# Optimization experiments

Hardware: AMD Instinct MI355X
Metric: run time of the kernel (lower is better)

The kernel has to match this reference:

```python
import jax, jax.numpy as jnp
import numpy as np

BS, NV, MF, MT, NP, K, NR = 8, 16, 16, 16, 8, 3, 12
H, NOUT = 64, 64


def setup_inputs() -> dict:
    key = jax.random.key(0)
    ks = jax.random.split(key, 8)
    rel_index = jax.random.uniform(ks[0], (BS, NV, MF, MT, NP, K, NR), jnp.float32)
    source_embed = jax.random.normal(ks[1], (BS, NV, MT, MF, H), jnp.float32)
    s = jax.random.normal(ks[2], (BS, NV, NOUT), jnp.float32)
    # relation matrices: W[0] is fixed all-ones, rest xavier_uniform(gain=1.414)
    bound = 1.414 * np.sqrt(6.0 / (H + H))
    W0 = jnp.ones((1, H, H), jnp.float32)
    Wr = jax.random.uniform(ks[3], (NR - 1, H, H), jnp.float32, -bound, bound)
    Wstack = jnp.concatenate([W0, Wr], axis=0)  # (NR, H, H)
    lb = 1.0 / np.sqrt(H + NOUT)
    lin_w = jax.random.uniform(ks[4], (1, H + NOUT), jnp.float32, -lb, lb)
    lin_b = jax.random.uniform(ks[5], (1,), jnp.float32, -lb, lb)
    ob = 1.0 / np.sqrt(H)
    out_w = jax.random.uniform(ks[6], (NOUT, H), jnp.float32, -ob, ob)
    out_b = jax.random.uniform(ks[7], (NOUT,), jnp.float32, -ob, ob)
    return dict(rel_index=rel_index, source_embed=source_embed, s=s,
                Wstack=Wstack, lin_w=lin_w, lin_b=lin_b, out_w=out_w, out_b=out_b)


def reference(rel_index, source_embed, s, Wstack, lin_w, lin_b, out_w, out_b):
    # Original: rels = (rel_index @ Wflat).view(..., K, h, h); W = prod over K (ELEMENTWISE);
    # einsum 'bvtfpdd,bvtfd->bvtfpd' takes the DIAGONAL of the (h,h) block.
    # diag(elementwise prod) == prod of diags, so only diag(W_r) is needed -> same math,
    # avoids materializing the (b,v,f,t,p,K,h,h) tensor.
    diag = jnp.diagonal(Wstack, axis1=-2, axis2=-1)              # (nr, h)
    rels_d = jnp.einsum('bvftpkr,rd->bvftpkd', rel_index, diag)  # (b,v,f,t,p,K,h)
    Wd = jnp.prod(rels_d, axis=-2)                               # prod over K -> (b,v,f,t,p,h)
    Wd = jnp.swapaxes(Wd, 2, 3)                                  # permute -> (b,v,t,f,p,h)
    z_j = Wd * source_embed[..., None, :]                        # (b,v,t,f,p,h)
    # attention: Linear(cat([s, z_j])) split into the two weight blocks (cat order: s first)
    nout = s.shape[-1]
    w_s, w_z = lin_w[0, :nout], lin_w[0, nout:]
    logits = (s @ w_s)[:, :, None, None, None] \
             + jnp.einsum('bvtfpd,d->bvtfp', z_j, w_z) + lin_b[0]  # (b,v,t,f,p)
    attn = jax.nn.softmax(logits, axis=-1)
    z = jnp.einsum('bvtfp,bvtfpd->bvtfd', attn, z_j)             # path-weighted aggregation
    # output_layer: Dropout (identity in eval) -> Linear -> ReLU
    out = jax.nn.relu(jnp.einsum('bvtfd,od->bvtfo', z, out_w) + out_b)
    return out.sum(axis=3).sum(axis=2)                           # sum over f then t -> (b,v,nout)
```

## Files before the change

kernel.cpp:

```cpp
#include <hip/hip_runtime.h>

namespace {
constexpr int kNP = 8, kNR = 12;
constexpr int kRelCell = 288;
constexpr int kH = 64, kNOUT = 64;
constexpr int CELLS = 4;
constexpr int WT_LD = 65;
}

__device__ __forceinline__ float readlane_f(float v, int l) {
    union { float f; int i; } u; u.f = v;
    u.i = __builtin_amdgcn_readlane(u.i, l);
    return u.f;
}

template<int CTRL>
__device__ __forceinline__ float dpp_add(float x) {
    int y = __builtin_amdgcn_update_dpp(0, __float_as_int(x), CTRL, 0xf, 0xf, true);
    return x + __int_as_float(y);
}
__device__ __forceinline__ float wave_sum63(float x) {
    x = dpp_add<0x111>(x);
    x = dpp_add<0x112>(x);
    x = dpp_add<0x114>(x);
    x = dpp_add<0x118>(x);
    x = dpp_add<0x142>(x);
    x = dpp_add<0x143>(x);
    return x;
}

__global__ __launch_bounds__(256, 4) void gal_kernel(
    const float* __restrict__ rel,
    const float* __restrict__ se,
    const float* __restrict__ s,
    const float* __restrict__ Wstack,
    const float* __restrict__ lin_w,
    const float* __restrict__ lin_b,
    const float* __restrict__ out_w,
    const float* __restrict__ out_b,
    float* __restrict__ out)
{
    __shared__ __align__(16) float wT[kH * WT_LD];
    __shared__ __align__(16) float dshare[kNR * kH];

    const int tid  = (int)threadIdx.x;
    const int lane = tid & 63;
    const int w    = __builtin_amdgcn_readfirstlane(tid >> 6);

    const int bv = (int)blockIdx.x >> 4;
    const int f  = (int)blockIdx.x & 15;
    const int t0 = w * CELLS;

    for (int i = tid; i < kH * kNOUT; i += 256) {
        const int o = i >> 6, d = i & 63;
        wT[d * WT_LD + o] = out_w[i];
    }
    for (int i = tid; i < kNR * kH; i += 256) {
        const int r = i >> 6, d = i & 63;
        dshare[i] = Wstack[r * kH * kH + d * (kH + 1)];
    }

    const float wz = lin_w[kNOUT + lane];
    const float ob = out_b[lane];
    const float* sep = se + ((size_t)(bv * 16 + t0) * 16 + f) * kH + lane;
    float sev[CELLS];
#pragma unroll
    for (int i = 0; i < CELLS; ++i) sev[i] = sep[(size_t)i * (16 * kH)];

    __syncthreads();
    float dreg[kNR];
#pragma unroll
    for (int r = 0; r < kNR; ++r) dreg[r] = dshare[r * kH + lane];
    __syncthreads();

    const float* relbase = rel + ((size_t)((bv * 16 + f) * 16) + t0) * kRelCell;

    float zreg[CELLS];
#pragma unroll
    for (int i = 0; i < CELLS; ++i) {
        const float* cb = relbase + (size_t)i * kRelCell;
        const float sv_i = sev[i];
        float zj[kNP], la[kNP];
#pragma unroll
        for (int p = 0; p < kNP; ++p) {
            const float4* r4 = (const float4*)(cb + p * 36);
            const float4 a0 = r4[0], a1 = r4[1], a2 = r4[2];
            const float4 b0 = r4[3], b1 = r4[4], b2 = r4[5];
            const float4 c0 = r4[6], c1 = r4[7], c2 = r4[8];
            float d0 = a0.x*dreg[0] + a0.y*dreg[1] + a0.z*dreg[2] + a0.w*dreg[3]
                     + a1.x*dreg[4] + a1.y*dreg[5] + a1.z*dreg[6] + a1.w*dreg[7]
                     + a2.x*dreg[8] + a2.y*dreg[9] + a2.z*dreg[10] + a2.w*dreg[11];
            float d1 = b0.x*dreg[0] + b0.y*dreg[1] + b0.z*dreg[2] + b0.w*dreg[3]
                     + b1.x*dreg[4] + b1.y*dreg[5] + b1.z*dreg[6] + b1.w*dreg[7]
                     + b2.x*dreg[8] + b2.y*dreg[9] + b2.z*dreg[10] + b2.w*dreg[11];
            float d2 = c0.x*dreg[0] + c0.y*dreg[1] + c0.z*dreg[2] + c0.w*dreg[3]
                     + c1.x*dreg[4] + c1.y*dreg[5] + c1.z*dreg[6] + c1.w*dreg[7]
                     + c2.x*dreg[8] + c2.y*dreg[9] + c2.z*dreg[10] + c2.w*dreg[11];
            const float z = d0 * d1 * d2 * sv_i;
            zj[p] = z;
            la[p] = z * wz;
        }
#pragma unroll
        for (int p = 0; p < kNP; ++p) la[p] = wave_sum63(la[p]);
        float lg[kNP];
#pragma unroll
        for (int p = 0; p < kNP; ++p) lg[p] = readlane_f(la[p], 63);
        float mx = lg[0];
#pragma unroll
        for (int p = 1; p < kNP; ++p) mx = fmaxf(mx, lg[p]);
        float esum = 0.f, zd = 0.f;
#pragma unroll
        for (int p = 0; p < kNP; ++p) {
            const float e = __expf(lg[p] - mx);
            esum += e;
            zd = fmaf(e, zj[p], zd);
        }
        zreg[i] = zd / esum;
    }

    float q[CELLS];
#pragma unroll
    for (int i = 0; i < CELLS; ++i) q[i] = 0.f;
#pragma unroll
    for (int d = 0; d < kH; ++d) {
        const float wv = wT[d * WT_LD + lane];
#pragma unroll
        for (int i = 0; i < CELLS; ++i)
            q[i] = fmaf(readlane_f(zreg[i], d), wv, q[i]);
    }
    float tot = 0.f;
#pragma unroll
    for (int i = 0; i < CELLS; ++i) tot += fmaxf(q[i] + ob, 0.f);

    dshare[w * 64 + lane] = tot;
    __syncthreads();
    if (w == 0) {
        const float r = dshare[lane] + dshare[64 + lane]
                      + dshare[128 + lane] + dshare[192 + lane];
        atomicAdd(&out[bv * kNOUT + lane], r);
    }
}

extern "C" void kernel_launch(void* const* d_in, const int* in_sizes, int n_in,
                              void* d_out, int out_size, void* d_ws, size_t ws_size,
                              hipStream_t stream) {
    const float* rel   = (const float*)d_in[0];
    const float* sem   = (const float*)d_in[1];
    const float* s     = (const float*)d_in[2];
    const float* Wst   = (const float*)d_in[3];
    const float* lin_w = (const float*)d_in[4];
    const float* lin_b = (const float*)d_in[5];
    const float* out_w = (const float*)d_in[6];
    const float* out_b = (const float*)d_in[7];
    float* out = (float*)d_out;

    hipMemsetAsync(out, 0, sizeof(float) * 8 * 16 * kNOUT, stream);
    dim3 grid(2048), block(256);
    hipLaunchKernelGGL(gal_kernel, grid, block, 0, stream,
                       rel, sem, s, Wst, lin_w, lin_b, out_w, out_b, out);
}
```

Measured before the change: 51.18 us.

## Stage rel cells into LDS via async global_load_lds and broadcast z via LDS

New measurement: 66.40 us. 1.3x slower.

```diff
diff --git a/kernel.cpp b/kernel.cpp
--- a/kernel.cpp
+++ b/kernel.cpp
@@ -5,6 +5,7 @@
 constexpr int kRelCell = 288;
 constexpr int kH = 64, kNOUT = 64;
 constexpr int CELLS = 4;
+constexpr int WAVES = 4;
 constexpr int WT_LD = 65;
 }
 
@@ -29,6 +30,57 @@
     return x;
 }
 
+__device__ __forceinline__ void gll16(const float* g, float* l) {
+    __builtin_amdgcn_global_load_lds(
+        (const __attribute__((address_space(1))) void*)g,
+        (__attribute__((address_space(3))) void*)l, 16, 0, 0);
+}
+__device__ __forceinline__ void stage_cell(const float* g, float* lds, int lane) {
+    gll16(g + lane * 4, lds);
+    if (lane < 8) gll16(g + 256 + lane * 4, lds + 256);
+}
+
+__device__ __forceinline__ float cell_z(const float* __restrict__ cb,
+                                        const float* __restrict__ dreg,
+                                        float sv_i, float wz) {
+    float zj[kNP], la[kNP];
+#pragma unroll
+    for (int p = 0; p < kNP; ++p) {
+        const float4* r4 = (const float4*)(cb + p * 36);
+        const float4 a0 = r4[0], a1 = r4[1], a2 = r4[2];
+        const float4 b0 = r4[3], b1 = r4[4], b2 = r4[5];
+        const float4 c0 = r4[6], c1 = r4[7], c2 = r4[8];
+        float d0 = a0.x*dreg[0] + a0.y*dreg[1] + a0.z*dreg[2] + a0.w*dreg[3]
+                 + a1.x*dreg[4] + a1.y*dreg[5] + a1.z*dreg[6] + a1.w*dreg[7]
+                 + a2.x*dreg[8] + a2.y*dreg[9] + a2.z*dreg[10] + a2.w*dreg[11];
+        float d1 = b0.x*dreg[0] + b0.y*dreg[1] + b0.z*dreg[2] + b0.w*dreg[3]
+                 + b1.x*dreg[4] + b1.y*dreg[5] + b1.z*dreg[6] + b1.w*dreg[7]
+                 + b2.x*dreg[8] + b2.y*dreg[9] + b2.z*dreg[10] + b2.w*dreg[11];
+        float d2 = c0.x*dreg[0] + c0.y*dreg[1] + c0.z*dreg[2] + c0.w*dreg[3]
+                 + c1.x*dreg[4] + c1.y*dreg[5] + c1.z*dreg[6] + c1.w*dreg[7]
+                 + c2.x*dreg[8] + c2.y*dreg[9] + c2.z*dreg[10] + c2.w*dreg[11];
+        const float z = d0 * d1 * d2 * sv_i;
+        zj[p] = z;
+        la[p] = z * wz;
+    }
+#pragma unroll
+    for (int p = 0; p < kNP; ++p) la[p] = wave_sum63(la[p]);
+    float lg[kNP];
+#pragma unroll
+    for (int p = 0; p < kNP; ++p) lg[p] = readlane_f(la[p], 63);
+    float mx = lg[0];
+#pragma unroll
+    for (int p = 1; p < kNP; ++p) mx = fmaxf(mx, lg[p]);
+    float esum = 0.f, zd = 0.f;
+#pragma unroll
+    for (int p = 0; p < kNP; ++p) {
+        const float e = __expf(lg[p] - mx);
+        esum += e;
+        zd = fmaf(e, zj[p], zd);
+    }
+    return zd / esum;
+}
+
 __global__ __launch_bounds__(256, 4) void gal_kernel(
     const float* __restrict__ rel,
     const float* __restrict__ se,
@@ -41,7 +93,7 @@
     float* __restrict__ out)
 {
     __shared__ __align__(16) float wT[kH * WT_LD];
-    __shared__ __align__(16) float dshare[kNR * kH];
+    __shared__ __align__(16) float relbuf[WAVES][2][kRelCell];
 
     const int tid  = (int)threadIdx.x;
     const int lane = tid & 63;
@@ -51,15 +103,20 @@
     const int f  = (int)blockIdx.x & 15;
     const int t0 = w * CELLS;
 
+    const float* relbase = rel + ((size_t)((bv * 16 + f) * 16) + t0) * kRelCell;
+
+    stage_cell(relbase,                &relbuf[w][0][0], lane);
+    stage_cell(relbase + 2 * kRelCell, &relbuf[w][1][0], lane);
+
     for (int i = tid; i < kH * kNOUT; i += 256) {
         const int o = i >> 6, d = i & 63;
         wT[d * WT_LD + o] = out_w[i];
     }
-    for (int i = tid; i < kNR * kH; i += 256) {
-        const int r = i >> 6, d = i & 63;
-        dshare[i] = Wstack[r * kH * kH + d * (kH + 1)];
-    }
 
+    float dreg[kNR];
+#pragma unroll
+    for (int r = 0; r < kNR; ++r)
+        dreg[r] = Wstack[r * kH * kH + lane * (kH + 1)];
     const float wz = lin_w[kNOUT + lane];
     const float ob = out_b[lane];
     const float* sep = se + ((size_t)(bv * 16 + t0) * 16 + f) * kH + lane;
@@ -68,55 +125,18 @@
     for (int i = 0; i < CELLS; ++i) sev[i] = sep[(size_t)i * (16 * kH)];
 
     __syncthreads();
-    float dreg[kNR];
-#pragma unroll
-    for (int r = 0; r < kNR; ++r) dreg[r] = dshare[r * kH + lane];
-    __syncthreads();
-
-    const float* relbase = rel + ((size_t)((bv * 16 + f) * 16) + t0) * kRelCell;
 
     float zreg[CELLS];
+    zreg[0] = cell_z(&relbuf[w][0][0],          dreg, sev[0], wz);
+    zreg[1] = cell_z(relbase + 1 * kRelCell,    dreg, sev[1], wz);
+    zreg[2] = cell_z(&relbuf[w][1][0],          dreg, sev[2], wz);
+    zreg[3] = cell_z(relbase + 3 * kRelCell,    dreg, sev[3], wz);
+
+    float* zb = &relbuf[w][0][0];
 #pragma unroll
-    for (int i = 0; i < CELLS; ++i) {
-        const float* cb = relbase + (size_t)i * kRelCell;
-        const float sv_i = sev[i];
-        float zj[kNP], la[kNP];
-#pragma unroll
-        for (int p = 0; p < kNP; ++p) {
-            const float4* r4 = (const float4*)(cb + p * 36);
-            const float4 a0 = r4[0], a1 = r4[1], a2 = r4[2];
-            const float4 b0 = r4[3], b1 = r4[4], b2 = r4[5];
-            const float4 c0 = r4[6], c1 = r4[7], c2 = r4[8];
-            float d0 = a0.x*dreg[0] + a0.y*dreg[1] + a0.z*dreg[2] + a0.w*dreg[3]
-                     + a1.x*dreg[4] + a1.y*dreg[5] + a1.z*dreg[6] + a1.w*dreg[7]
-                     + a2.x*dreg[8] + a2.y*dreg[9] + a2.z*dreg[10] + a2.w*dreg[11];
-            float d1 = b0.x*dreg[0] + b0.y*dreg[1] + b0.z*dreg[2] + b0.w*dreg[3]
-                     + b1.x*dreg[4] + b1.y*dreg[5] + b1.z*dreg[6] + b1.w*dreg[7]
-                     + b2.x*dreg[8] + b2.y*dreg[9] + b2.z*dreg[10] + b2.w*dreg[11];
-            float d2 = c0.x*dreg[0] + c0.y*dreg[1] + c0.z*dreg[2] + c0.w*dreg[3]
-                     + c1.x*dreg[4] + c1.y*dreg[5] + c1.z*dreg[6] + c1.w*dreg[7]
-                     + c2.x*dreg[8] + c2.y*dreg[9] + c2.z*dreg[10] + c2.w*dreg[11];
-            const float z = d0 * d1 * d2 * sv_i;
-            zj[p] = z;
-            la[p] = z * wz;
-        }
-#pragma unroll
-        for (int p = 0; p < kNP; ++p) la[p] = wave_sum63(la[p]);
-        float lg[kNP];
-#pragma unroll
-        for (int p = 0; p < kNP; ++p) lg[p] = readlane_f(la[p], 63);
-        float mx = lg[0];
-#pragma unroll
-        for (int p = 1; p < kNP; ++p) mx = fmaxf(mx, lg[p]);
-        float esum = 0.f, zd = 0.f;
-#pragma unroll
-        for (int p = 0; p < kNP; ++p) {
-            const float e = __expf(lg[p] - mx);
-            esum += e;
-            zd = fmaf(e, zj[p], zd);
-        }
-        zreg[i] = zd / esum;
-    }
+    for (int i = 0; i < CELLS; ++i) zb[lane * 4 + i] = zreg[i];
+    asm volatile("s_waitcnt lgkmcnt(0)" ::: "memory");
+    __builtin_amdgcn_sched_barrier(0);
 
     float q[CELLS];
 #pragma unroll
@@ -124,19 +144,21 @@
 #pragma unroll
     for (int d = 0; d < kH; ++d) {
         const float wv = wT[d * WT_LD + lane];
-#pragma unroll
-        for (int i = 0; i < CELLS; ++i)
-            q[i] = fmaf(readlane_f(zreg[i], d), wv, q[i]);
+        const float4 zv = *(const float4*)&zb[d * 4];
+        q[0] = fmaf(zv.x, wv, q[0]);
+        q[1] = fmaf(zv.y, wv, q[1]);
+        q[2] = fmaf(zv.z, wv, q[2]);
+        q[3] = fmaf(zv.w, wv, q[3]);
     }
     float tot = 0.f;
 #pragma unroll
     for (int i = 0; i < CELLS; ++i) tot += fmaxf(q[i] + ob, 0.f);
 
-    dshare[w * 64 + lane] = tot;
+    relbuf[w][1][lane] = tot;
     __syncthreads();
     if (w == 0) {
-        const float r = dshare[lane] + dshare[64 + lane]
-                      + dshare[128 + lane] + dshare[192 + lane];
+        const float r = relbuf[0][1][lane] + relbuf[1][1][lane]
+                      + relbuf[2][1][lane] + relbuf[3][1][lane];
         atomicAdd(&out[bv * kNOUT + lane], r);
     }
 }
```
